# Kernel optimization log

Hardware: AMD Instinct MI355X
Metric: run time of the kernel (lower is better)

The kernel has to match this reference:

```python
import jax, jax.numpy as jnp
import numpy as np
from jax import lax


def rgb2hsl(rgb):
    # rgb: [B,3,H,W] in [0,1]
    cmax = jnp.max(rgb, axis=1, keepdims=True)
    cmin = jnp.min(rgb, axis=1, keepdims=True)
    amax = jnp.argmax(rgb, axis=1, keepdims=True)  # first-occurrence, like torch.max
    delta = cmax - cmin
    idx = jnp.where(delta == 0, 3, amax)
    safe_d = jnp.where(delta == 0, 1.0, delta)
    r, g, b = rgb[:, 0:1], rgb[:, 1:2], rgb[:, 2:3]
    h0 = jnp.mod((g - b) / safe_d, 6.0)
    h1 = (b - r) / safe_d + 2.0
    h2 = (r - g) / safe_d + 4.0
    hsl_h = jnp.where(idx == 0, h0,
            jnp.where(idx == 1, h1,
            jnp.where(idx == 2, h2, 0.0))) / 6.0
    hsl_l = (cmax + cmin) / 2.0
    # s = delta/(2l) if l<=0.5 else delta/(2-2l); 0 at l==0 or l==1
    denom = jnp.where(hsl_l <= 0.5, 2.0 * hsl_l, 2.0 - 2.0 * hsl_l)
    safe_den = jnp.where(denom == 0, 1.0, denom)
    in_range = (hsl_l > 0) & (hsl_l < 1)
    hsl_s = jnp.where(in_range, delta / safe_den, 0.0)
    return jnp.concatenate([hsl_h, hsl_s, hsl_l], axis=1)


def conv2d_same(x, w, b):
    y = lax.conv_general_dilated(x, w, window_strides=(1, 1), padding='SAME',
                                 dimension_numbers=('NCHW', 'OIHW', 'NCHW'))
    return y + b[None, :, None, None]


def setup_inputs() -> dict:
    key = jax.random.key(0)
    k = jax.random.split(key, 5)
    B, H, W = 32, 512, 512
    KS = 5
    fan1 = 1 * KS * KS
    fan2 = 2 * KS * KS
    return {
        'x': jax.random.uniform(k[0], (B, 3, H, W), dtype=jnp.float32),
        'w1': jax.random.normal(k[1], (3, 1, KS, KS), dtype=jnp.float32) / np.sqrt(fan1),
        'b1': jax.random.normal(k[2], (3,), dtype=jnp.float32) * 0.01,
        'w2': jax.random.normal(k[3], (3, 2, KS, KS), dtype=jnp.float32) / np.sqrt(fan2),
        'b2': jax.random.normal(k[4], (3,), dtype=jnp.float32) * 0.01,
    }


def reference(x, w1, b1, w2, b2):
    x_hsl = rgb2hsl(x)
    xl = conv2d_same(x_hsl[:, 2:3], w1, b1)   # L plane -> conv1
    xr = conv2d_same(x_hsl[:, 0:2], w2, b2)   # H,S planes -> conv2
    return (xl, xr)
```

## Files before the change

### kernel.cpp

```cpp
#include <hip/hip_runtime.h>

typedef _Float16 h2 __attribute__((ext_vector_type(2)));

__device__ __forceinline__ float fd2(unsigned a, unsigned b, float c) {
  return __builtin_amdgcn_fdot2(__builtin_bit_cast(h2, a), __builtin_bit_cast(h2, b), c, false);
}
__device__ __forceinline__ unsigned pkrtz(float a, float b) {
  return __builtin_bit_cast(unsigned, __builtin_amdgcn_cvt_pkrtz(a, b));
}

#define TW 64
#define TH 32
#define ROWS 36
#define SWW 84
#define SLW 88

__global__ __launch_bounds__(256, 6) void fused_hsl_conv(
    const float* __restrict__ x,
    const float* __restrict__ w1,
    const float* __restrict__ b1,
    const float* __restrict__ w2,
    const float* __restrict__ b2,
    float* __restrict__ out,
    int B)
{
  __shared__ unsigned sHS[ROWS][SWW];
  __shared__ __align__(16) _Float16 sL[ROWS][SLW];
  __shared__ unsigned swHS[5][16];
  __shared__ unsigned swL[5][16];

  const int tid = threadIdx.x;

  if (tid < 15) {
    const int o = tid % 3, dy = tid / 3;
    #pragma unroll
    for (int dx = 0; dx < 5; ++dx)
      swHS[dy][o * 5 + dx] = pkrtz(w2[o * 50 + dy * 5 + dx],
                                   w2[o * 50 + 25 + dy * 5 + dx]);
  } else if (tid >= 32 && tid < 47) {
    const int t2 = tid - 32, o = t2 % 3, dy = t2 / 3;
    float wv[5];
    #pragma unroll
    for (int dx = 0; dx < 5; ++dx) wv[dx] = w1[o * 25 + dy * 5 + dx];
    swL[dy][o * 3 + 0] = pkrtz(wv[0], wv[1]);
    swL[dy][o * 3 + 1] = pkrtz(wv[2], wv[3]);
    swL[dy][o * 3 + 2] = pkrtz(wv[4], 0.f);
  } else if (tid >= 64 && tid < 69) {
    swHS[tid - 64][15] = 0;
  } else if (tid >= 96 && tid < 131) {
    const int t3 = tid - 96;
    swL[t3 / 7][9 + t3 % 7] = 0;
  }

  const int nwg = gridDim.x;
  const int bsw = (blockIdx.x & 7) * (nwg >> 3) + (blockIdx.x >> 3);
  const int ty0 = (bsw & 15) * TH;
  const int tx0 = ((bsw >> 4) & 7) * TW;
  const int b   = bsw >> 7;

  const size_t pln = 512 * 512;
  const float* pr = x + (size_t)b * 3 * pln;
  const float* pg = pr + pln;
  const float* pb = pg + pln;

  float4 Rv[3], Gv[3], Bv[3];
  int rowA[3], tA[3];
  const bool act = tid < 216;
  #pragma unroll
  for (int k = 0; k < 3; ++k) {
    const int i = k * 216 + tid;
    const int row = i / 18, t = i - row * 18;
    rowA[k] = row; tA[k] = t;
    const int gy = ty0 - 2 + row;
    const int gx0 = tx0 - 4 + 4 * t;
    Rv[k] = make_float4(0.f, 0.f, 0.f, 0.f);
    Gv[k] = Rv[k]; Bv[k] = Rv[k];
    if (act && gy >= 0 && gy < 512 && gx0 >= 0 && gx0 < 512) {
      const size_t off = (size_t)gy * 512 + gx0;
      Rv[k] = *(const float4*)(pr + off);
      Gv[k] = *(const float4*)(pg + off);
      Bv[k] = *(const float4*)(pb + off);
    }
  }
  #pragma unroll
  for (int k = 0; k < 3; ++k) {
    const int row = rowA[k], t = tA[k];
    const float ra[4] = {Rv[k].x, Rv[k].y, Rv[k].z, Rv[k].w};
    const float ga[4] = {Gv[k].x, Gv[k].y, Gv[k].z, Gv[k].w};
    const float ba[4] = {Bv[k].x, Bv[k].y, Bv[k].z, Bv[k].w};
    unsigned hs[4]; _Float16 lv[4];
    #pragma unroll
    for (int p = 0; p < 4; ++p) {
      const float r = ra[p], g = ga[p], bl = ba[p];
      const float cmax = fmaxf(r, fmaxf(g, bl));
      const float cmin = fminf(r, fminf(g, bl));
      const float delta = cmax - cmin;
      const float l = 0.5f * (cmax + cmin);
      const float rd = __builtin_amdgcn_rcpf(delta);
      float h0 = (g - bl) * rd;
      h0 = (h0 < 0.f) ? h0 + 6.f : h0;
      const float h1v = (bl - r) * rd + 2.f;
      const float h2v = (r - g) * rd + 4.f;
      float hv = (r >= g && r >= bl) ? h0 : ((g >= bl) ? h1v : h2v);
      const float h = (delta != 0.f) ? hv * (1.f / 6.f) : 0.f;
      const float denom = (l <= 0.5f) ? (2.f * l) : (2.f - 2.f * l);
      const float s = (delta != 0.f && l > 0.f && l < 1.f)
                        ? delta * __builtin_amdgcn_rcpf(denom) : 0.f;
      hs[p] = pkrtz(h, s);
      lv[p] = (_Float16)l;
    }
    if (act) {
      if (t >= 1)  *(uint2*)&sHS[row][4 * t - 2] = make_uint2(hs[0], hs[1]);
      if (t <= 16) *(uint2*)&sHS[row][4 * t]     = make_uint2(hs[2], hs[3]);
      unsigned* rl = (unsigned*)&sL[row][0];
      if (t >= 1)  rl[2 * t - 1] = __builtin_bit_cast(unsigned, (h2){lv[0], lv[1]});
      if (t <= 16) rl[2 * t]     = __builtin_bit_cast(unsigned, (h2){lv[2], lv[3]});
    }
  }
  if (tid < 72) ((unsigned*)&sL[tid >> 1][0])[34 + (tid & 1)] = 0;
  __syncthreads();

  const int lx = tid & 7;
  const int ly = tid >> 3;
  const int q0 = 8 * lx;

  float* outl = out + (size_t)b * 3 * pln;
  float* outr = out + ((size_t)B + b) * 3 * pln;
  const size_t ob = (size_t)(ty0 + ly) * 512 + (tx0 + q0);

  {
    float acc[3][8];
    const float b2v[3] = {b2[0], b2[1], b2[2]};
    #pragma unroll
    for (int o = 0; o < 3; ++o)
      #pragma unroll
      for (int p = 0; p < 8; ++p) acc[o][p] = b2v[o];

    #pragma unroll
    for (int dy = 0; dy < 5; ++dy) {
      const unsigned* rowp = &sHS[ly + dy][0];
      const uint4 A0 = *(const uint4*)(rowp + q0);
      const uint4 A1 = *(const uint4*)(rowp + q0 + 4);
      const uint4 A2 = *(const uint4*)(rowp + q0 + 8);
      const unsigned hw[12] = {A0.x, A0.y, A0.z, A0.w, A1.x, A1.y, A1.z, A1.w,
                               A2.x, A2.y, A2.z, A2.w};
      const uint4 W0 = *(const uint4*)&swHS[dy][0];
      const uint4 W1 = *(const uint4*)&swHS[dy][4];
      const uint4 W2 = *(const uint4*)&swHS[dy][8];
      const uint4 W3 = *(const uint4*)&swHS[dy][12];
      const unsigned wt[15] = {W0.x, W0.y, W0.z, W0.w, W1.x, W1.y, W1.z, W1.w,
                               W2.x, W2.y, W2.z, W2.w, W3.x, W3.y, W3.z};
      #pragma unroll
      for (int o = 0; o < 3; ++o)
        #pragma unroll
        for (int p = 0; p < 8; ++p)
          #pragma unroll
          for (int dx = 0; dx < 5; ++dx)
            acc[o][p] = fd2(hw[p + dx], wt[o * 5 + dx], acc[o][p]);
    }
    #pragma unroll
    for (int o = 0; o < 3; ++o) {
      *(float4*)(outr + o * pln + ob)     = make_float4(acc[o][0], acc[o][1], acc[o][2], acc[o][3]);
      *(float4*)(outr + o * pln + ob + 4) = make_float4(acc[o][4], acc[o][5], acc[o][6], acc[o][7]);
    }
  }

  {
    float acc[3][8];
    const float b1v[3] = {b1[0], b1[1], b1[2]};
    #pragma unroll
    for (int o = 0; o < 3; ++o)
      #pragma unroll
      for (int p = 0; p < 8; ++p) acc[o][p] = b1v[o];

    #pragma unroll
    for (int dy = 0; dy < 5; ++dy) {
      const unsigned* rowp = (const unsigned*)&sL[ly + dy][0];
      const uint4 L0 = *(const uint4*)(rowp + 4 * lx);
      const uint4 L1 = *(const uint4*)(rowp + 4 * lx + 4);
      const unsigned w[8] = {L0.x, L0.y, L0.z, L0.w, L1.x, L1.y, L1.z, L1.w};
      unsigned s[6];
      #pragma unroll
      for (int k = 0; k < 6; ++k)
        s[k] = __builtin_amdgcn_alignbit(w[k + 1], w[k], 16);
      const uint4 V0 = *(const uint4*)&swL[dy][0];
      const uint4 V1 = *(const uint4*)&swL[dy][4];
      const unsigned c8 = swL[dy][8];
      const unsigned wt[9] = {V0.x, V0.y, V0.z, V0.w, V1.x, V1.y, V1.z, V1.w, c8};
      #pragma unroll
      for (int o = 0; o < 3; ++o)
        #pragma unroll
        for (int p = 0; p < 8; ++p) {
          const int hh = p >> 1;
          const unsigned* src = (p & 1) ? s : w;
          acc[o][p] = fd2(src[hh],     wt[o * 3 + 0], acc[o][p]);
          acc[o][p] = fd2(src[hh + 1], wt[o * 3 + 1], acc[o][p]);
          acc[o][p] = fd2(src[hh + 2], wt[o * 3 + 2], acc[o][p]);
        }
    }
    #pragma unroll
    for (int o = 0; o < 3; ++o) {
      *(float4*)(outl + o * pln + ob)     = make_float4(acc[o][0], acc[o][1], acc[o][2], acc[o][3]);
      *(float4*)(outl + o * pln + ob + 4) = make_float4(acc[o][4], acc[o][5], acc[o][6], acc[o][7]);
    }
  }
}

extern "C" void kernel_launch(void* const* d_in, const int* in_sizes, int n_in,
                              void* d_out, int out_size, void* d_ws, size_t ws_size,
                              hipStream_t stream) {
  const float* x  = (const float*)d_in[0];
  const float* w1 = (const float*)d_in[1];
  const float* b1 = (const float*)d_in[2];
  const float* w2 = (const float*)d_in[3];
  const float* b2 = (const float*)d_in[4];
  float* out = (float*)d_out;

  const int B = in_sizes[0] / (3 * 512 * 512);
  const int grid = B * 8 * 16;
  fused_hsl_conv<<<grid, 256, 0, stream>>>(x, w1, b1, w2, b2, out, B);
}
```

Measured before the change: 76.80 us.

## Make blocks persistent over four row tiles with double-buffered prefetch

Each workgroup now processes four vertically stacked 64x32 tiles instead of one. The next tile's RGB loads are issued before computing the current tile's convolutions, and converted into a second LDS buffer afterward, so global load latency overlaps compute. The goal is to hide memory latency and amortize weight/bias setup. In exchange, LDS use doubles, the grid shrinks by a factor of four, occupancy is lowered to 4 waves per SIMD hint, and register pressure rises from the prefetched values.

```diff
diff --git a/kernel.cpp b/kernel.cpp
--- a/kernel.cpp
+++ b/kernel.cpp
@@ -14,8 +14,9 @@
 #define ROWS 36
 #define SWW 84
 #define SLW 88
-
-__global__ __launch_bounds__(256, 6) void fused_hsl_conv(
+#define NT 4
+
+__global__ __launch_bounds__(256, 4) void fused_hsl_conv(
     const float* __restrict__ x,
     const float* __restrict__ w1,
     const float* __restrict__ b1,
@@ -24,8 +25,8 @@
     float* __restrict__ out,
     int B)
 {
-  __shared__ unsigned sHS[ROWS][SWW];
-  __shared__ __align__(16) _Float16 sL[ROWS][SLW];
+  __shared__ unsigned sHS[2][ROWS][SWW];
+  __shared__ __align__(16) _Float16 sL[2][ROWS][SLW];
   __shared__ unsigned swHS[5][16];
   __shared__ unsigned swL[5][16];
 
@@ -51,158 +52,181 @@
     const int t3 = tid - 96;
     swL[t3 / 7][9 + t3 % 7] = 0;
   }
+  if (tid < 72) {
+    const int r = tid >> 1, w = 34 + (tid & 1);
+    ((unsigned*)&sL[0][r][0])[w] = 0;
+    ((unsigned*)&sL[1][r][0])[w] = 0;
+  }
 
   const int nwg = gridDim.x;
   const int bsw = (blockIdx.x & 7) * (nwg >> 3) + (blockIdx.x >> 3);
-  const int ty0 = (bsw & 15) * TH;
-  const int tx0 = ((bsw >> 4) & 7) * TW;
-  const int b   = bsw >> 7;
+  const int b   = bsw >> 5;
+  const int rem = bsw & 31;
+  const int tx0 = (rem & 7) * TW;
+  const int tyb = (rem >> 3) * (NT * TH);
 
   const size_t pln = 512 * 512;
   const float* pr = x + (size_t)b * 3 * pln;
   const float* pg = pr + pln;
   const float* pb = pg + pln;
-
-  float4 Rv[3], Gv[3], Bv[3];
+  float* outl = out + (size_t)b * 3 * pln;
+  float* outr = out + ((size_t)B + b) * 3 * pln;
+
+  const float b1v0 = b1[0], b1v1 = b1[1], b1v2 = b1[2];
+  const float b2v0 = b2[0], b2v1 = b2[1], b2v2 = b2[2];
+
+  const bool act = tid < 216;
   int rowA[3], tA[3];
-  const bool act = tid < 216;
   #pragma unroll
   for (int k = 0; k < 3; ++k) {
     const int i = k * 216 + tid;
-    const int row = i / 18, t = i - row * 18;
-    rowA[k] = row; tA[k] = t;
-    const int gy = ty0 - 2 + row;
-    const int gx0 = tx0 - 4 + 4 * t;
-    Rv[k] = make_float4(0.f, 0.f, 0.f, 0.f);
-    Gv[k] = Rv[k]; Bv[k] = Rv[k];
-    if (act && gy >= 0 && gy < 512 && gx0 >= 0 && gx0 < 512) {
-      const size_t off = (size_t)gy * 512 + gx0;
-      Rv[k] = *(const float4*)(pr + off);
-      Gv[k] = *(const float4*)(pg + off);
-      Bv[k] = *(const float4*)(pb + off);
-    }
-  }
-  #pragma unroll
-  for (int k = 0; k < 3; ++k) {
-    const int row = rowA[k], t = tA[k];
-    const float ra[4] = {Rv[k].x, Rv[k].y, Rv[k].z, Rv[k].w};
-    const float ga[4] = {Gv[k].x, Gv[k].y, Gv[k].z, Gv[k].w};
-    const float ba[4] = {Bv[k].x, Bv[k].y, Bv[k].z, Bv[k].w};
-    unsigned hs[4]; _Float16 lv[4];
-    #pragma unroll
-    for (int p = 0; p < 4; ++p) {
-      const float r = ra[p], g = ga[p], bl = ba[p];
-      const float cmax = fmaxf(r, fmaxf(g, bl));
-      const float cmin = fminf(r, fminf(g, bl));
-      const float delta = cmax - cmin;
-      const float l = 0.5f * (cmax + cmin);
-      const float rd = __builtin_amdgcn_rcpf(delta);
-      float h0 = (g - bl) * rd;
-      h0 = (h0 < 0.f) ? h0 + 6.f : h0;
-      const float h1v = (bl - r) * rd + 2.f;
-      const float h2v = (r - g) * rd + 4.f;
-      float hv = (r >= g && r >= bl) ? h0 : ((g >= bl) ? h1v : h2v);
-      const float h = (delta != 0.f) ? hv * (1.f / 6.f) : 0.f;
-      const float denom = (l <= 0.5f) ? (2.f * l) : (2.f - 2.f * l);
-      const float s = (delta != 0.f && l > 0.f && l < 1.f)
-                        ? delta * __builtin_amdgcn_rcpf(denom) : 0.f;
-      hs[p] = pkrtz(h, s);
-      lv[p] = (_Float16)l;
-    }
-    if (act) {
-      if (t >= 1)  *(uint2*)&sHS[row][4 * t - 2] = make_uint2(hs[0], hs[1]);
-      if (t <= 16) *(uint2*)&sHS[row][4 * t]     = make_uint2(hs[2], hs[3]);
-      unsigned* rl = (unsigned*)&sL[row][0];
-      if (t >= 1)  rl[2 * t - 1] = __builtin_bit_cast(unsigned, (h2){lv[0], lv[1]});
-      if (t <= 16) rl[2 * t]     = __builtin_bit_cast(unsigned, (h2){lv[2], lv[3]});
-    }
-  }
-  if (tid < 72) ((unsigned*)&sL[tid >> 1][0])[34 + (tid & 1)] = 0;
-  __syncthreads();
+    rowA[k] = i / 18;
+    tA[k]   = i - rowA[k] * 18;
+  }
+
+  auto issue_loads = [&](int ty0, float4* Rv, float4* Gv, float4* Bv) {
+    #pragma unroll
+    for (int k = 0; k < 3; ++k) {
+      const int gy  = ty0 - 2 + rowA[k];
+      const int gx0 = tx0 - 4 + 4 * tA[k];
+      Rv[k] = make_float4(0.f, 0.f, 0.f, 0.f);
+      Gv[k] = Rv[k]; Bv[k] = Rv[k];
+      if (act && gy >= 0 && gy < 512 && gx0 >= 0 && gx0 < 512) {
+        const size_t off = (size_t)gy * 512 + gx0;
+        Rv[k] = *(const float4*)(pr + off);
+        Gv[k] = *(const float4*)(pg + off);
+        Bv[k] = *(const float4*)(pb + off);
+      }
+    }
+  };
+
+  auto convert_store = [&](int buf, const float4* Rv, const float4* Gv, const float4* Bv) {
+    #pragma unroll
+    for (int k = 0; k < 3; ++k) {
+      const int row = rowA[k], t = tA[k];
+      const float ra[4] = {Rv[k].x, Rv[k].y, Rv[k].z, Rv[k].w};
+      const float ga[4] = {Gv[k].x, Gv[k].y, Gv[k].z, Gv[k].w};
+      const float ba[4] = {Bv[k].x, Bv[k].y, Bv[k].z, Bv[k].w};
+      unsigned hs[4]; _Float16 lv[4];
+      #pragma unroll
+      for (int p = 0; p < 4; ++p) {
+        const float r = ra[p], g = ga[p], bl = ba[p];
+        const float cmax = fmaxf(r, fmaxf(g, bl));
+        const float cmin = fminf(r, fminf(g, bl));
+        const float delta = cmax - cmin;
+        const float l = 0.5f * (cmax + cmin);
+        const float rd = __builtin_amdgcn_rcpf(delta);
+        float h0 = (g - bl) * rd;
+        h0 = (h0 < 0.f) ? h0 + 6.f : h0;
+        const float h1v = (bl - r) * rd + 2.f;
+        const float h2v = (r - g) * rd + 4.f;
+        float hv = (r >= g && r >= bl) ? h0 : ((g >= bl) ? h1v : h2v);
+        const float h = (delta != 0.f) ? hv * (1.f / 6.f) : 0.f;
+        const float denom = (l <= 0.5f) ? (2.f * l) : (2.f - 2.f * l);
+        const float s = (delta != 0.f && l > 0.f && l < 1.f)
+                          ? delta * __builtin_amdgcn_rcpf(denom) : 0.f;
+        hs[p] = pkrtz(h, s);
+        lv[p] = (_Float16)l;
+      }
+      if (act) {
+        if (t >= 1)  *(uint2*)&sHS[buf][row][4 * t - 2] = make_uint2(hs[0], hs[1]);
+        if (t <= 16) *(uint2*)&sHS[buf][row][4 * t]     = make_uint2(hs[2], hs[3]);
+        unsigned* rl = (unsigned*)&sL[buf][row][0];
+        if (t >= 1)  rl[2 * t - 1] = __builtin_bit_cast(unsigned, (h2){lv[0], lv[1]});
+        if (t <= 16) rl[2 * t]     = __builtin_bit_cast(unsigned, (h2){lv[2], lv[3]});
+      }
+    }
+  };
 
   const int lx = tid & 7;
   const int ly = tid >> 3;
   const int q0 = 8 * lx;
 
-  float* outl = out + (size_t)b * 3 * pln;
-  float* outr = out + ((size_t)B + b) * 3 * pln;
-  const size_t ob = (size_t)(ty0 + ly) * 512 + (tx0 + q0);
-
-  {
-    float acc[3][8];
-    const float b2v[3] = {b2[0], b2[1], b2[2]};
-    #pragma unroll
-    for (int o = 0; o < 3; ++o)
-      #pragma unroll
-      for (int p = 0; p < 8; ++p) acc[o][p] = b2v[o];
-
-    #pragma unroll
-    for (int dy = 0; dy < 5; ++dy) {
-      const unsigned* rowp = &sHS[ly + dy][0];
-      const uint4 A0 = *(const uint4*)(rowp + q0);
-      const uint4 A1 = *(const uint4*)(rowp + q0 + 4);
-      const uint4 A2 = *(const uint4*)(rowp + q0 + 8);
-      const unsigned hw[12] = {A0.x, A0.y, A0.z, A0.w, A1.x, A1.y, A1.z, A1.w,
-                               A2.x, A2.y, A2.z, A2.w};
-      const uint4 W0 = *(const uint4*)&swHS[dy][0];
-      const uint4 W1 = *(const uint4*)&swHS[dy][4];
-      const uint4 W2 = *(const uint4*)&swHS[dy][8];
-      const uint4 W3 = *(const uint4*)&swHS[dy][12];
-      const unsigned wt[15] = {W0.x, W0.y, W0.z, W0.w, W1.x, W1.y, W1.z, W1.w,
-                               W2.x, W2.y, W2.z, W2.w, W3.x, W3.y, W3.z};
-      #pragma unroll
-      for (int o = 0; o < 3; ++o)
+  float4 Rv[3], Gv[3], Bv[3];
+  issue_loads(tyb, Rv, Gv, Bv);
+  convert_store(0, Rv, Gv, Bv);
+  __syncthreads();
+
+  for (int it = 0; it < NT; ++it) {
+    const int ty0 = tyb + it * TH;
+    const int buf = it & 1;
+
+    float4 Rn[3], Gn[3], Bn[3];
+    if (it + 1 < NT) issue_loads(ty0 + TH, Rn, Gn, Bn);
+
+    const size_t ob = (size_t)(ty0 + ly) * 512 + (tx0 + q0);
+
+    {
+      float acc[3][8];
+      #pragma unroll
+      for (int p = 0; p < 8; ++p) { acc[0][p] = b2v0; acc[1][p] = b2v1; acc[2][p] = b2v2; }
+      #pragma unroll
+      for (int dy = 0; dy < 5; ++dy) {
+        const unsigned* rowp = &sHS[buf][ly + dy][0];
+        const uint4 A0 = *(const uint4*)(rowp + q0);
+        const uint4 A1 = *(const uint4*)(rowp + q0 + 4);
+        const uint4 A2 = *(const uint4*)(rowp + q0 + 8);
+        const unsigned hw[12] = {A0.x, A0.y, A0.z, A0.w, A1.x, A1.y, A1.z, A1.w,
+                                 A2.x, A2.y, A2.z, A2.w};
+        const uint4 W0 = *(const uint4*)&swHS[dy][0];
+        const uint4 W1 = *(const uint4*)&swHS[dy][4];
+        const uint4 W2 = *(const uint4*)&swHS[dy][8];
+        const uint4 W3 = *(const uint4*)&swHS[dy][12];
+        const unsigned wt[15] = {W0.x, W0.y, W0.z, W0.w, W1.x, W1.y, W1.z, W1.w,
+                                 W2.x, W2.y, W2.z, W2.w, W3.x, W3.y, W3.z};
         #pragma unroll
-        for (int p = 0; p < 8; ++p)
+        for (int o = 0; o < 3; ++o)
           #pragma unroll
-          for (int dx = 0; dx < 5; ++dx)
-            acc[o][p] = fd2(hw[p + dx], wt[o * 5 + dx], acc[o][p]);
-    }
-    #pragma unroll
-    for (int o = 0; o < 3; ++o) {
-      *(float4*)(outr + o * pln + ob)     = make_float4(acc[o][0], acc[o][1], acc[o][2], acc[o][3]);
-      *(float4*)(outr + o * pln + ob + 4) = make_float4(acc[o][4], acc[o][5], acc[o][6], acc[o][7]);
-    }
-  }
-
-  {
-    float acc[3][8];
-    const float b1v[3] = {b1[0], b1[1], b1[2]};
-    #pragma unroll
-    for (int o = 0; o < 3; ++o)
-      #pragma unroll
-      for (int p = 0; p < 8; ++p) acc[o][p] = b1v[o];
-
-    #pragma unroll
-    for (int dy = 0; dy < 5; ++dy) {
-      const unsigned* rowp = (const unsigned*)&sL[ly + dy][0];
-      const uint4 L0 = *(const uint4*)(rowp + 4 * lx);
-      const uint4 L1 = *(const uint4*)(rowp + 4 * lx + 4);
-      const unsigned w[8] = {L0.x, L0.y, L0.z, L0.w, L1.x, L1.y, L1.z, L1.w};
-      unsigned s[6];
-      #pragma unroll
-      for (int k = 0; k < 6; ++k)
-        s[k] = __builtin_amdgcn_alignbit(w[k + 1], w[k], 16);
-      const uint4 V0 = *(const uint4*)&swL[dy][0];
-      const uint4 V1 = *(const uint4*)&swL[dy][4];
-      const unsigned c8 = swL[dy][8];
-      const unsigned wt[9] = {V0.x, V0.y, V0.z, V0.w, V1.x, V1.y, V1.z, V1.w, c8};
-      #pragma unroll
-      for (int o = 0; o < 3; ++o)
+          for (int p = 0; p < 8; ++p)
+            #pragma unroll
+            for (int dx = 0; dx < 5; ++dx)
+              acc[o][p] = fd2(hw[p + dx], wt[o * 5 + dx], acc[o][p]);
+      }
+      #pragma unroll
+      for (int o = 0; o < 3; ++o) {
+        *(float4*)(outr + o * pln + ob)     = make_float4(acc[o][0], acc[o][1], acc[o][2], acc[o][3]);
+        *(float4*)(outr + o * pln + ob + 4) = make_float4(acc[o][4], acc[o][5], acc[o][6], acc[o][7]);
+      }
+    }
+
+    {
+      float acc[3][8];
+      #pragma unroll
+      for (int p = 0; p < 8; ++p) { acc[0][p] = b1v0; acc[1][p] = b1v1; acc[2][p] = b1v2; }
+      #pragma unroll
+      for (int dy = 0; dy < 5; ++dy) {
+        const unsigned* rowp = (const unsigned*)&sL[buf][ly + dy][0];
+        const uint4 L0 = *(const uint4*)(rowp + 4 * lx);
+        const uint4 L1 = *(const uint4*)(rowp + 4 * lx + 4);
+        const unsigned w[8] = {L0.x, L0.y, L0.z, L0.w, L1.x, L1.y, L1.z, L1.w};
+        unsigned s[6];
         #pragma unroll
-        for (int p = 0; p < 8; ++p) {
-          const int hh = p >> 1;
-          const unsigned* src = (p & 1) ? s : w;
-          acc[o][p] = fd2(src[hh],     wt[o * 3 + 0], acc[o][p]);
-          acc[o][p] = fd2(src[hh + 1], wt[o * 3 + 1], acc[o][p]);
-          acc[o][p] = fd2(src[hh + 2], wt[o * 3 + 2], acc[o][p]);
-        }
-    }
-    #pragma unroll
-    for (int o = 0; o < 3; ++o) {
-      *(float4*)(outl + o * pln + ob)     = make_float4(acc[o][0], acc[o][1], acc[o][2], acc[o][3]);
-      *(float4*)(outl + o * pln + ob + 4) = make_float4(acc[o][4], acc[o][5], acc[o][6], acc[o][7]);
-    }
+        for (int k = 0; k < 6; ++k)
+          s[k] = __builtin_amdgcn_alignbit(w[k + 1], w[k], 16);
+        const uint4 V0 = *(const uint4*)&swL[dy][0];
+        const uint4 V1 = *(const uint4*)&swL[dy][4];
+        const unsigned c8 = swL[dy][8];
+        const unsigned wt[9] = {V0.x, V0.y, V0.z, V0.w, V1.x, V1.y, V1.z, V1.w, c8};
+        #pragma unroll
+        for (int o = 0; o < 3; ++o)
+          #pragma unroll
+          for (int p = 0; p < 8; ++p) {
+            const int hh = p >> 1;
+            const unsigned* src = (p & 1) ? s : w;
+            acc[o][p] = fd2(src[hh],     wt[o * 3 + 0], acc[o][p]);
+            acc[o][p] = fd2(src[hh + 1], wt[o * 3 + 1], acc[o][p]);
+            acc[o][p] = fd2(src[hh + 2], wt[o * 3 + 2], acc[o][p]);
+          }
+      }
+      #pragma unroll
+      for (int o = 0; o < 3; ++o) {
+        *(float4*)(outl + o * pln + ob)     = make_float4(acc[o][0], acc[o][1], acc[o][2], acc[o][3]);
+        *(float4*)(outl + o * pln + ob + 4) = make_float4(acc[o][4], acc[o][5], acc[o][6], acc[o][7]);
+      }
+    }
+
+    if (it + 1 < NT) convert_store(buf ^ 1, Rn, Gn, Bn);
+    __syncthreads();
   }
 }
 
@@ -217,6 +241,6 @@
   float* out = (float*)d_out;
 
   const int B = in_sizes[0] / (3 * 512 * 512);
-  const int grid = B * 8 * 16;
+  const int grid = B * 32;
   fused_hsl_conv<<<grid, 256, 0, stream>>>(x, w1, b1, w2, b2, out, B);
 }
```

New measurement: 73.41 us. 4.4% less time.
